# Kernel optimization log

Hardware: AMD Instinct MI355X
Metric: run time of the kernel (lower is better)

## Reference

```python
import jax, jax.numpy as jnp
import numpy as np

N_NODES = 10242  # icosphere level-5 node count
NNZ = 71694      # ~7 nonzeros per row (6 neighbors + self)


def setup_inputs() -> dict:
    key = jax.random.key(0)
    k1, k2, k3, k4, k5 = jax.random.split(key, 5)
    B, T, C, Cout, Ks = 2, 16, 16, 32, 20
    x = jax.random.normal(k1, (B, T, N_NODES, C), dtype=jnp.float32)
    edge_row = jax.random.randint(k2, (NNZ,), 0, N_NODES, dtype=jnp.int32)
    edge_col = jax.random.randint(k3, (NNZ,), 0, N_NODES, dtype=jnp.int32)
    # small values keep the Chebyshev recurrence numerically bounded over Ks steps
    edge_val = jax.random.uniform(k4, (NNZ,), dtype=jnp.float32, minval=-0.2, maxval=0.2)
    W = jax.random.normal(k5, (Cout, C * Ks), dtype=jnp.float32) * 0.02
    return {"x": x, "edge_row": edge_row, "edge_col": edge_col,
            "edge_val": edge_val, "W": W}


def reference(x, edge_row, edge_col, edge_val, W):
    B, T, N, C = x.shape
    Cout, CK = W.shape
    Ks = CK // C

    def spmm(v):  # sparse L @ v, v: [N, F]
        return jax.ops.segment_sum(edge_val[:, None] * v[edge_col], edge_row,
                                   num_segments=N)

    # [B,T,N,C] -> [B*T,N,C] -> [N,C,B*T] -> [N, C*B*T]
    x0 = x.reshape(B * T, N, C).transpose(1, 2, 0).reshape(N, C * B * T)
    x1 = spmm(x0)

    def step(carry, _):
        a, b = carry
        c = 2.0 * spmm(b) - a
        return (b, c), c

    _, rest = jax.lax.scan(step, (x0, x1), None, length=Ks - 2)
    xs = jnp.concatenate([x0[None], x1[None], rest], axis=0)  # [Ks, N, C*B*T]

    xs = xs.reshape(Ks, N, C, B * T).transpose(3, 1, 2, 0)  # [B*T, N, C, Ks]
    xs = xs.reshape(B * T * N, C * Ks)
    out = xs @ W.T  # [B*T*N, Cout]
    return out.reshape(B, T, N, Cout)
```

## Files before the change

kernel.cpp:

```cpp
#include <hip/hip_runtime.h>

#define N_NODES 10242
#define NNZ_E   71694
#define NNZ_PAD_MAX (NNZ_E + 7 * N_NODES + 64)
#define BT      32
#define C_IN    16
#define K_S     20
#define C_OUT   32
#define F       512
typedef unsigned short u16;
typedef unsigned int   u32;

#define RING_ELEMS ((size_t)N_NODES * F)
#define RING_BYTES (RING_ELEMS * 2)

#define NSLICE  8
#define SLICE_U16 (F / NSLICE)

typedef __attribute__((ext_vector_type(8)))  _Float16 half8;
typedef __attribute__((ext_vector_type(16))) float    float16;

__device__ __forceinline__ void unpack8h(uint4 u, float* f) {
    union { uint4 u; _Float16 h[8]; } v; v.u = u;
    #pragma unroll
    for (int i = 0; i < 8; ++i) f[i] = (float)v.h[i];
}
__device__ __forceinline__ uint4 pack8h(const float* f) {
    union { uint4 u; _Float16 h[8]; } v;
    #pragma unroll
    for (int i = 0; i < 8; ++i) v.h[i] = (_Float16)f[i];
    return v.u;
}
__device__ __forceinline__ u16 f2h(float f) {
    union { _Float16 h; u16 u; } v; v.h = (_Float16)f; return v.u;
}


__global__ __launch_bounds__(256) void init_kernel(
        const float* __restrict__ W, int* __restrict__ cnt,
        u16* __restrict__ wtfrag) {
    int i = blockIdx.x * 256 + threadIdx.x;
    if (i < N_NODES) cnt[i] = 0;
    int w = i - N_NODES;
    if (w >= 0 && w < K_S * 64 * 8) {
        int j    = w & 7;
        int lane = (w >> 3) & 63;
        int k    = w >> 9;
        int cout = lane & 31;
        int c    = ((lane >> 5) << 3) + j;
        wtfrag[w] = f2h(W[cout * (C_IN * K_S) + c * K_S + k]);
    }
}

__global__ __launch_bounds__(256) void count_kernel(
        const int* __restrict__ erow, int* cnt) {
    int e = blockIdx.x * 256 + threadIdx.x;
    if (e < NNZ_E) atomicAdd(&cnt[erow[e]], 1);
}

__global__ __launch_bounds__(256) void scan_kernel(
        const int* __restrict__ cnt, int* row_ptr, int* cursor) {
    const int T = 256;
    const int chunk = (N_NODES + T - 1) / T;
    __shared__ int part[T];
    int t = threadIdx.x;
    int base = t * chunk;
    int s = 0;
    for (int i = 0; i < chunk; ++i) {
        int idx = base + i;
        if (idx < N_NODES) s += (cnt[idx] + 7) & ~7;
    }
    part[t] = s;
    __syncthreads();
    for (int off = 1; off < T; off <<= 1) {
        int v = (t >= off) ? part[t - off] : 0;
        __syncthreads();
        part[t] += v;
        __syncthreads();
    }
    int run = (t == 0) ? 0 : part[t - 1];
    for (int i = 0; i < chunk; ++i) {
        int idx = base + i;
        if (idx < N_NODES) {
            row_ptr[idx] = run;
            cursor[idx]  = run;
            run += (cnt[idx] + 7) & ~7;
        }
    }
    if (t == T - 1) row_ptr[N_NODES] = part[T - 1];
}

__global__ __launch_bounds__(256) void scatter_kernel(
        const int* __restrict__ erow, const int* __restrict__ ecol,
        const float* __restrict__ eval, int* cursor, int2* __restrict__ cpack) {
    int e = blockIdx.x * 256 + threadIdx.x;
    if (e < NNZ_E) {
        int p = atomicAdd(&cursor[erow[e]], 1);
        cpack[p] = make_int2(ecol[e], __float_as_int(eval[e]));
    }
}

__global__ __launch_bounds__(256) void finalize_kernel(
        const int* __restrict__ row_ptr, const int* __restrict__ cursor,
        int2* cpack) {
    int r = blockIdx.x * 256 + threadIdx.x;
    if (r >= N_NODES) return;
    int sbeg = row_ptr[r];
    int send = cursor[r];
    int pend = row_ptr[r + 1];
    for (int i = sbeg + 1; i < send; ++i) {
        int2 key = cpack[i];
        int j = i - 1;
        while (j >= sbeg) {
            int2 q = cpack[j];
            bool gt = (q.x > key.x) || (q.x == key.x && (u32)q.y > (u32)key.y);
            if (!gt) break;
            cpack[j + 1] = q;
            --j;
        }
        cpack[j + 1] = key;
    }
    for (int p = send; p < pend; ++p) cpack[p] = make_int2(0, 0);
}


__global__ __launch_bounds__(256) void transform_kernel(
        const float* __restrict__ x, u16* __restrict__ T0) {
    int g = blockIdx.x * 256 + threadIdx.x;
    int n   = g >> 9;
    int rem = g & 511;
    int bt  = rem >> 4;
    int c   = rem & 15;
    float v = x[((size_t)bt * N_NODES + n) * C_IN + c];
    T0[(size_t)n * F + rem] = f2h(v);
}


__global__ __launch_bounds__(256) void spmm_slice_kernel(
        const u16* __restrict__ srcB, const u16* __restrict__ srcA,
        u16* __restrict__ dst,
        const int* __restrict__ row_ptr, const int2* __restrict__ cpack,
        float alpha, float beta) {
    const int slice = blockIdx.x & 7;
    const int chunk = blockIdx.x >> 3;
    const int wave  = threadIdx.x >> 6;
    const int lane  = threadIdx.x & 63;
    const int l     = lane & 7;
    const int n     = chunk * 32 + wave * 8 + (lane >> 3);
    const bool valid = (n < N_NODES);

    const int s   = valid ? row_ptr[n] : 0;
    const int len = valid ? (row_ptr[n + 1] - s) : 0;

    const size_t soff = (size_t)slice * SLICE_U16 + (size_t)l * 8;

    float a[8] = {0,0,0,0,0,0,0,0};
    if (beta != 0.f && valid) {
        uint4 ua = *(const uint4*)(srcA + (size_t)n * F + soff);
        unpack8h(ua, a);
    }

    float acc[8] = {0,0,0,0,0,0,0,0};
    const int gbase = lane & 56;

    for (int c = 0; c * 8 < len; ++c) {
        int2 my = cpack[s + c * 8 + l];
        int col[8]; float v[8];
        #pragma unroll
        for (int r = 0; r < 8; ++r) {
            col[r] = __shfl(my.x, gbase + r, 64);
            v[r]   = __int_as_float(__shfl(my.y, gbase + r, 64));
        }
        uint4 g0 = *(const uint4*)(srcB + (size_t)col[0] * F + soff);
        uint4 g1 = *(const uint4*)(srcB + (size_t)col[1] * F + soff);
        uint4 g2 = *(const uint4*)(srcB + (size_t)col[2] * F + soff);
        uint4 g3 = *(const uint4*)(srcB + (size_t)col[3] * F + soff);
        uint4 g4 = *(const uint4*)(srcB + (size_t)col[4] * F + soff);
        uint4 g5 = *(const uint4*)(srcB + (size_t)col[5] * F + soff);
        uint4 g6 = *(const uint4*)(srcB + (size_t)col[6] * F + soff);
        uint4 g7 = *(const uint4*)(srcB + (size_t)col[7] * F + soff);
        float b0[8], b1[8], b2[8], b3[8], b4[8], b5[8], b6[8], b7[8];
        unpack8h(g0, b0); unpack8h(g1, b1); unpack8h(g2, b2); unpack8h(g3, b3);
        unpack8h(g4, b4); unpack8h(g5, b5); unpack8h(g6, b6); unpack8h(g7, b7);
        #pragma unroll
        for (int i = 0; i < 8; ++i) {
            acc[i] += v[0] * b0[i];
            acc[i] += v[1] * b1[i];
            acc[i] += v[2] * b2[i];
            acc[i] += v[3] * b3[i];
            acc[i] += v[4] * b4[i];
            acc[i] += v[5] * b5[i];
            acc[i] += v[6] * b6[i];
            acc[i] += v[7] * b7[i];
        }
    }

    if (valid) {
        float y[8];
        #pragma unroll
        for (int i = 0; i < 8; ++i)
            y[i] = alpha * acc[i] + beta * a[i];
        *(uint4*)(dst + (size_t)n * F + soff) = pack8h(y);
    }
}


__global__ __launch_bounds__(256) void proj_mfma_kernel(
        const u16* __restrict__ ring, int R, int k0, int kcnt,
        const u16* __restrict__ wtfrag, float* __restrict__ out, int accumulate) {
    const int lane = threadIdx.x & 63;
    const int n = (blockIdx.x << 2) + (threadIdx.x >> 6);
    if (n >= N_NODES) return;
    const int col = lane & 31;
    const int grp = lane >> 5;
    const size_t aoff = (size_t)n * F + (size_t)col * 16 + grp * 8;

    union U { uint4 u; half8 h; };
    float16 acc0 = {};
    float16 acc1 = {};
    int j = 0;
    for (; j + 2 <= kcnt; j += 2) {
        int ka = k0 + j, kb = k0 + j + 1;
        U a0, b0, a1, b1;
        a0.u = *(const uint4*)(ring + (size_t)(ka % R) * RING_ELEMS + aoff);
        b0.u = *(const uint4*)(wtfrag + (size_t)ka * 512 + lane * 8);
        a1.u = *(const uint4*)(ring + (size_t)(kb % R) * RING_ELEMS + aoff);
        b1.u = *(const uint4*)(wtfrag + (size_t)kb * 512 + lane * 8);
        acc0 = __builtin_amdgcn_mfma_f32_32x32x16_f16(a0.h, b0.h, acc0, 0, 0, 0);
        acc1 = __builtin_amdgcn_mfma_f32_32x32x16_f16(a1.h, b1.h, acc1, 0, 0, 0);
    }
    if (j < kcnt) {
        int ka = k0 + j;
        U a0, b0;
        a0.u = *(const uint4*)(ring + (size_t)(ka % R) * RING_ELEMS + aoff);
        b0.u = *(const uint4*)(wtfrag + (size_t)ka * 512 + lane * 8);
        acc0 = __builtin_amdgcn_mfma_f32_32x32x16_f16(a0.h, b0.h, acc0, 0, 0, 0);
    }

    #pragma unroll
    for (int r = 0; r < 16; ++r) {
        int bt = (r & 3) + 8 * (r >> 2) + 4 * grp;
        float* op = out + ((size_t)bt * N_NODES + n) * C_OUT + col;
        float val = acc0[r] + acc1[r];
        if (accumulate) *op += val;
        else            *op  = val;
    }
}


extern "C" void kernel_launch(void* const* d_in, const int* in_sizes, int n_in,
                              void* d_out, int out_size, void* d_ws, size_t ws_size,
                              hipStream_t stream) {
    const float* x    = (const float*)d_in[0];
    const int*   erow = (const int*)  d_in[1];
    const int*   ecol = (const int*)  d_in[2];
    const float* eval = (const float*)d_in[3];
    const float* W    = (const float*)d_in[4];
    float* out = (float*)d_out;

    char* ws = (char*)d_ws;
    size_t o = 0;
    auto alloc = [&](size_t bytes) -> char* {
        o = (o + 511) & ~(size_t)511;
        char* r = ws + o;
        o += bytes;
        return r;
    };
    int*   cnt     = (int*)  alloc((size_t)N_NODES * 4);
    int*   row_ptr = (int*)  alloc((size_t)(N_NODES + 1) * 4);
    int*   cursor  = (int*)  alloc((size_t)N_NODES * 4);
    int2*  cpack   = (int2*) alloc((size_t)NNZ_PAD_MAX * 8);
    u16*   wtfrag  = (u16*)  alloc((size_t)K_S * 512 * 2);

    o = (o + 511) & ~(size_t)511;
    int R = (int)((ws_size - o) / RING_BYTES);
    if (R > K_S) R = K_S;
    if (R < 3)  R = 3;
    u16* ring = (u16*)(ws + o);
    auto slot = [&](int k) -> u16* { return ring + (size_t)(k % R) * RING_ELEMS; };

    init_kernel<<<(N_NODES + K_S * 512 + 255) / 256, 256, 0, stream>>>(W, cnt, wtfrag);
    count_kernel<<<(NNZ_E + 255) / 256, 256, 0, stream>>>(erow, cnt);
    scan_kernel<<<1, 256, 0, stream>>>(cnt, row_ptr, cursor);
    scatter_kernel<<<(NNZ_E + 255) / 256, 256, 0, stream>>>(erow, ecol, eval, cursor, cpack);
    finalize_kernel<<<(N_NODES + 255) / 256, 256, 0, stream>>>(row_ptr, cursor, cpack);

    const int grid4  = (N_NODES + 3) / 4;
    const int gridsl = NSLICE * ((N_NODES + 31) / 32);
    int c0 = 0;
    auto maybe_pass = [&](int k_done) {
        int target = K_S - c0;
        if (target > R) target = R;
        if (target > 0 && (k_done - c0 + 1) == target) {
            proj_mfma_kernel<<<grid4, 256, 0, stream>>>(
                ring, R, c0, target, wtfrag, out, (c0 > 0) ? 1 : 0);
            c0 += target;
        }
    };

    transform_kernel<<<(int)(RING_ELEMS / 256), 256, 0, stream>>>(x, slot(0));
    maybe_pass(0);

    for (int k = 1; k < K_S; ++k) {
        const u16* srcB = slot(k - 1);
        const u16* srcA = (k >= 2) ? slot(k - 2) : slot(k - 1);
        float alpha = (k == 1) ? 1.f : 2.f;
        float beta  = (k == 1) ? 0.f : -1.f;
        spmm_slice_kernel<<<gridsl, 256, 0, stream>>>(
            srcB, srcA, slot(k), row_ptr, cpack, alpha, beta);
        maybe_pass(k);
    }
}
```

Measured before the change: 451.0 us.

## Run whole Chebyshev recurrence per feature pair in LDS-resident single kernel

Adds a chain kernel in which each of 256 blocks owns two feature columns, keeps the full node vector for two consecutive recurrence steps in shared memory, and runs all Ks-1 SpMM steps with block barriers. This replaces 19 separate SpMM launches that gathered from global memory. Edges are repacked into 32-bit words holding a 16-bit column and an fp16 value, and nodes are sorted by row-length class to reduce divergence. A single projection pass follows when the workspace ring holds all Ks slots. The cost is about 80KB of LDS per block, which limits occupancy, scattered fp16 writes to the ring, and fp16 rounding of the edge values.

```diff
diff --git a/kernel.cpp b/kernel.cpp
--- a/kernel.cpp
+++ b/kernel.cpp
@@ -33,6 +33,15 @@
 }
 __device__ __forceinline__ u16 f2h(float f) {
     union { _Float16 h; u16 u; } v; v.h = (_Float16)f; return v.u;
+}
+__device__ __forceinline__ float h2f_lo(u32 w) {
+    union { u32 u; _Float16 h[2]; } v; v.u = w; return (float)v.h[0];
+}
+__device__ __forceinline__ float h2f_hi(u32 w) {
+    union { u32 u; _Float16 h[2]; } v; v.u = w; return (float)v.h[1];
+}
+__device__ __forceinline__ u32 packh2(float a, float b) {
+    union { u32 u; _Float16 h[2]; } v; v.h[0] = (_Float16)a; v.h[1] = (_Float16)b; return v.u;
 }
 
 
@@ -59,16 +68,26 @@
 }
 
 __global__ __launch_bounds__(256) void scan_kernel(
-        const int* __restrict__ cnt, int* row_ptr, int* cursor) {
+        const int* __restrict__ cnt, int* row_ptr, int* cursor,
+        int* class_cursor) {
     const int T = 256;
     const int chunk = (N_NODES + T - 1) / T;
     __shared__ int part[T];
+    __shared__ int ccnt[8];
     int t = threadIdx.x;
+    if (t < 8) ccnt[t] = 0;
+    __syncthreads();
     int base = t * chunk;
     int s = 0;
     for (int i = 0; i < chunk; ++i) {
         int idx = base + i;
-        if (idx < N_NODES) s += (cnt[idx] + 7) & ~7;
+        if (idx < N_NODES) {
+            int pl = (cnt[idx] + 7) & ~7;
+            s += pl;
+            int cls = (pl == 0) ? 0 : ((pl >> 3) - 1);
+            if (cls > 7) cls = 7;
+            atomicAdd(&ccnt[cls], 1);
+        }
     }
     part[t] = s;
     __syncthreads();
@@ -88,6 +107,11 @@
         }
     }
     if (t == T - 1) row_ptr[N_NODES] = part[T - 1];
+    __syncthreads();
+    if (t == 0) {
+        int r2 = 0;
+        for (int c2 = 0; c2 < 8; ++c2) { class_cursor[c2] = r2; r2 += ccnt[c2]; }
+    }
 }
 
 __global__ __launch_bounds__(256) void scatter_kernel(
@@ -102,7 +126,7 @@
 
 __global__ __launch_bounds__(256) void finalize_kernel(
         const int* __restrict__ row_ptr, const int* __restrict__ cursor,
-        int2* cpack) {
+        int2* cpack, u32* __restrict__ epack) {
     int r = blockIdx.x * 256 + threadIdx.x;
     if (r >= N_NODES) return;
     int sbeg = row_ptr[r];
@@ -121,86 +145,77 @@
         cpack[j + 1] = key;
     }
     for (int p = send; p < pend; ++p) cpack[p] = make_int2(0, 0);
-}
-
-
-__global__ __launch_bounds__(256) void transform_kernel(
-        const float* __restrict__ x, u16* __restrict__ T0) {
-    int g = blockIdx.x * 256 + threadIdx.x;
-    int n   = g >> 9;
-    int rem = g & 511;
-    int bt  = rem >> 4;
-    int c   = rem & 15;
-    float v = x[((size_t)bt * N_NODES + n) * C_IN + c];
-    T0[(size_t)n * F + rem] = f2h(v);
-}
-
-
-__global__ __launch_bounds__(256) void spmm_slice_kernel(
-        const u16* __restrict__ srcB, const u16* __restrict__ srcA,
-        u16* __restrict__ dst,
-        const int* __restrict__ row_ptr, const int2* __restrict__ cpack,
-        float alpha, float beta) {
-    const int slice = blockIdx.x & 7;
-    const int chunk = blockIdx.x >> 3;
-    const int wave  = threadIdx.x >> 6;
-    const int lane  = threadIdx.x & 63;
-    const int l     = lane & 7;
-    const int n     = chunk * 32 + wave * 8 + (lane >> 3);
-    const bool valid = (n < N_NODES);
-
-    const int s   = valid ? row_ptr[n] : 0;
-    const int len = valid ? (row_ptr[n + 1] - s) : 0;
-
-    const size_t soff = (size_t)slice * SLICE_U16 + (size_t)l * 8;
-
-    float a[8] = {0,0,0,0,0,0,0,0};
-    if (beta != 0.f && valid) {
-        uint4 ua = *(const uint4*)(srcA + (size_t)n * F + soff);
-        unpack8h(ua, a);
-    }
-
-    float acc[8] = {0,0,0,0,0,0,0,0};
-    const int gbase = lane & 56;
-
-    for (int c = 0; c * 8 < len; ++c) {
-        int2 my = cpack[s + c * 8 + l];
-        int col[8]; float v[8];
-        #pragma unroll
-        for (int r = 0; r < 8; ++r) {
-            col[r] = __shfl(my.x, gbase + r, 64);
-            v[r]   = __int_as_float(__shfl(my.y, gbase + r, 64));
-        }
-        uint4 g0 = *(const uint4*)(srcB + (size_t)col[0] * F + soff);
-        uint4 g1 = *(const uint4*)(srcB + (size_t)col[1] * F + soff);
-        uint4 g2 = *(const uint4*)(srcB + (size_t)col[2] * F + soff);
-        uint4 g3 = *(const uint4*)(srcB + (size_t)col[3] * F + soff);
-        uint4 g4 = *(const uint4*)(srcB + (size_t)col[4] * F + soff);
-        uint4 g5 = *(const uint4*)(srcB + (size_t)col[5] * F + soff);
-        uint4 g6 = *(const uint4*)(srcB + (size_t)col[6] * F + soff);
-        uint4 g7 = *(const uint4*)(srcB + (size_t)col[7] * F + soff);
-        float b0[8], b1[8], b2[8], b3[8], b4[8], b5[8], b6[8], b7[8];
-        unpack8h(g0, b0); unpack8h(g1, b1); unpack8h(g2, b2); unpack8h(g3, b3);
-        unpack8h(g4, b4); unpack8h(g5, b5); unpack8h(g6, b6); unpack8h(g7, b7);
-        #pragma unroll
-        for (int i = 0; i < 8; ++i) {
-            acc[i] += v[0] * b0[i];
-            acc[i] += v[1] * b1[i];
-            acc[i] += v[2] * b2[i];
-            acc[i] += v[3] * b3[i];
-            acc[i] += v[4] * b4[i];
-            acc[i] += v[5] * b5[i];
-            acc[i] += v[6] * b6[i];
-            acc[i] += v[7] * b7[i];
-        }
-    }
-
-    if (valid) {
-        float y[8];
-        #pragma unroll
-        for (int i = 0; i < 8; ++i)
-            y[i] = alpha * acc[i] + beta * a[i];
-        *(uint4*)(dst + (size_t)n * F + soff) = pack8h(y);
+    for (int p = sbeg; p < pend; ++p) {
+        int2 q = cpack[p];
+        epack[p] = ((u32)q.x & 0xFFFFu) |
+                   ((u32)f2h(__int_as_float(q.y)) << 16);
+    }
+}
+
+__global__ __launch_bounds__(256) void order_kernel(
+        const int* __restrict__ row_ptr, int* class_cursor,
+        int* __restrict__ node_order) {
+    int n = blockIdx.x * 256 + threadIdx.x;
+    if (n >= N_NODES) return;
+    int pl = row_ptr[n + 1] - row_ptr[n];
+    int cls = (pl == 0) ? 0 : ((pl >> 3) - 1);
+    if (cls > 7) cls = 7;
+    int pos = atomicAdd(&class_cursor[cls], 1);
+    node_order[pos] = n;
+}
+
+
+__global__ __launch_bounds__(1024) void chain_kernel(
+        const float* __restrict__ x, const int* __restrict__ row_ptr,
+        const u32* __restrict__ epack, const int* __restrict__ node_order,
+        u16* __restrict__ ring) {
+    __shared__ u32 Tsh[2][N_NODES];
+    const int t  = threadIdx.x;
+    const int b  = blockIdx.x;
+    const int f0 = ((b & 7) << 6) | ((b >> 3) << 1);
+    const int bt = f0 >> 4;
+    const int c0 = f0 & 15;
+
+    for (int i = t; i < N_NODES; i += 1024) {
+        const float* xp = x + ((size_t)bt * N_NODES + i) * C_IN + c0;
+        float2 xv = *(const float2*)xp;
+        u32 p = packh2(xv.x, xv.y);
+        Tsh[0][i] = p;
+        *(u32*)(ring + (size_t)i * F + f0) = p;
+    }
+    __syncthreads();
+
+    int cur = 0;
+    for (int k = 1; k < K_S; ++k) {
+        const u32* bsrc = &Tsh[cur][0];
+        u32* adst = &Tsh[cur ^ 1][0];
+        u16* rk = ring + (size_t)k * RING_ELEMS;
+        const float alpha = (k == 1) ? 1.f : 2.f;
+        const bool hasA = (k >= 2);
+        for (int i = t; i < N_NODES; i += 1024) {
+            int n = node_order[i];
+            int s = row_ptr[n], e = row_ptr[n + 1];
+            float a0 = 0.f, a1 = 0.f;
+            if (hasA) { u32 ap = adst[n]; a0 = h2f_lo(ap); a1 = h2f_hi(ap); }
+            float acc0 = 0.f, acc1 = 0.f;
+            for (int p = s; p < e; p += 8) {
+                uint4 q0 = *(const uint4*)(epack + p);
+                uint4 q1 = *(const uint4*)(epack + p + 4);
+                #define EDGE(u) { u32 cc = (u) & 0xFFFFu; u32 d = bsrc[cc]; \
+                    float vv = h2f_hi(u); \
+                    acc0 += vv * h2f_lo(d); acc1 += vv * h2f_hi(d); }
+                EDGE(q0.x) EDGE(q0.y) EDGE(q0.z) EDGE(q0.w)
+                EDGE(q1.x) EDGE(q1.y) EDGE(q1.z) EDGE(q1.w)
+                #undef EDGE
+            }
+            float y0 = alpha * acc0 - (hasA ? a0 : 0.f);
+            float y1 = alpha * acc1 - (hasA ? a1 : 0.f);
+            u32 yp = packh2(y0, y1);
+            adst[n] = yp;
+            *(u32*)(rk + (size_t)n * F + f0) = yp;
+        }
+        __syncthreads();
+        cur ^= 1;
     }
 }
 
@@ -248,6 +263,67 @@
 }
 
 
+__global__ __launch_bounds__(256) void transform_kernel(
+        const float* __restrict__ x, u16* __restrict__ T0) {
+    int g = blockIdx.x * 256 + threadIdx.x;
+    int n   = g >> 9;
+    int rem = g & 511;
+    int bt  = rem >> 4;
+    int c   = rem & 15;
+    float v = x[((size_t)bt * N_NODES + n) * C_IN + c];
+    T0[(size_t)n * F + rem] = f2h(v);
+}
+
+__global__ __launch_bounds__(256) void spmm_slice_kernel(
+        const u16* __restrict__ srcB, const u16* __restrict__ srcA,
+        u16* __restrict__ dst,
+        const int* __restrict__ row_ptr, const int2* __restrict__ cpack,
+        float alpha, float beta) {
+    const int slice = blockIdx.x & 7;
+    const int chunk = blockIdx.x >> 3;
+    const int wave  = threadIdx.x >> 6;
+    const int lane  = threadIdx.x & 63;
+    const int l     = lane & 7;
+    const int n     = chunk * 32 + wave * 8 + (lane >> 3);
+    const bool valid = (n < N_NODES);
+
+    const int s   = valid ? row_ptr[n] : 0;
+    const int len = valid ? (row_ptr[n + 1] - s) : 0;
+    const size_t soff = (size_t)slice * SLICE_U16 + (size_t)l * 8;
+
+    float a[8] = {0,0,0,0,0,0,0,0};
+    if (beta != 0.f && valid) {
+        uint4 ua = *(const uint4*)(srcA + (size_t)n * F + soff);
+        unpack8h(ua, a);
+    }
+    float acc[8] = {0,0,0,0,0,0,0,0};
+    const int gbase = lane & 56;
+    for (int c = 0; c * 8 < len; ++c) {
+        int2 my = cpack[s + c * 8 + l];
+        int col[8]; float v[8];
+        #pragma unroll
+        for (int r = 0; r < 8; ++r) {
+            col[r] = __shfl(my.x, gbase + r, 64);
+            v[r]   = __int_as_float(__shfl(my.y, gbase + r, 64));
+        }
+        #pragma unroll
+        for (int r = 0; r < 8; ++r) {
+            uint4 g = *(const uint4*)(srcB + (size_t)col[r] * F + soff);
+            float bb[8];
+            unpack8h(g, bb);
+            #pragma unroll
+            for (int i = 0; i < 8; ++i) acc[i] += v[r] * bb[i];
+        }
+    }
+    if (valid) {
+        float y[8];
+        #pragma unroll
+        for (int i = 0; i < 8; ++i) y[i] = alpha * acc[i] + beta * a[i];
+        *(uint4*)(dst + (size_t)n * F + soff) = pack8h(y);
+    }
+}
+
+
 extern "C" void kernel_launch(void* const* d_in, const int* in_sizes, int n_in,
                               void* d_out, int out_size, void* d_ws, size_t ws_size,
                               hipStream_t stream) {
@@ -266,11 +342,14 @@
         o += bytes;
         return r;
     };
-    int*   cnt     = (int*)  alloc((size_t)N_NODES * 4);
-    int*   row_ptr = (int*)  alloc((size_t)(N_NODES + 1) * 4);
-    int*   cursor  = (int*)  alloc((size_t)N_NODES * 4);
-    int2*  cpack   = (int2*) alloc((size_t)NNZ_PAD_MAX * 8);
-    u16*   wtfrag  = (u16*)  alloc((size_t)K_S * 512 * 2);
+    int*   cnt      = (int*)  alloc((size_t)N_NODES * 4);
+    int*   row_ptr  = (int*)  alloc((size_t)(N_NODES + 1) * 4);
+    int*   cursor   = (int*)  alloc((size_t)N_NODES * 4);
+    int2*  cpack    = (int2*) alloc((size_t)NNZ_PAD_MAX * 8);
+    u32*   epack    = (u32*)  alloc((size_t)NNZ_PAD_MAX * 4);
+    u16*   wtfrag   = (u16*)  alloc((size_t)K_S * 512 * 2);
+    int*   clscur   = (int*)  alloc(8 * 4);
+    int*   norder   = (int*)  alloc((size_t)N_NODES * 4);
 
     o = (o + 511) & ~(size_t)511;
     int R = (int)((ws_size - o) / RING_BYTES);
@@ -281,11 +360,20 @@
 
     init_kernel<<<(N_NODES + K_S * 512 + 255) / 256, 256, 0, stream>>>(W, cnt, wtfrag);
     count_kernel<<<(NNZ_E + 255) / 256, 256, 0, stream>>>(erow, cnt);
-    scan_kernel<<<1, 256, 0, stream>>>(cnt, row_ptr, cursor);
+    scan_kernel<<<1, 256, 0, stream>>>(cnt, row_ptr, cursor, clscur);
     scatter_kernel<<<(NNZ_E + 255) / 256, 256, 0, stream>>>(erow, ecol, eval, cursor, cpack);
-    finalize_kernel<<<(N_NODES + 255) / 256, 256, 0, stream>>>(row_ptr, cursor, cpack);
-
-    const int grid4  = (N_NODES + 3) / 4;
+    finalize_kernel<<<(N_NODES + 255) / 256, 256, 0, stream>>>(row_ptr, cursor, cpack, epack);
+    order_kernel<<<(N_NODES + 255) / 256, 256, 0, stream>>>(row_ptr, clscur, norder);
+
+    const int grid4 = (N_NODES + 3) / 4;
+
+    if (R >= K_S) {
+        chain_kernel<<<256, 1024, 0, stream>>>(x, row_ptr, epack, norder, ring);
+        proj_mfma_kernel<<<grid4, 256, 0, stream>>>(
+            ring, K_S, 0, K_S, wtfrag, out, 0);
+        return;
+    }
+
     const int gridsl = NSLICE * ((N_NODES + 31) / 32);
     int c0 = 0;
     auto maybe_pass = [&](int k_done) {
@@ -297,10 +385,8 @@
             c0 += target;
         }
     };
-
     transform_kernel<<<(int)(RING_ELEMS / 256), 256, 0, stream>>>(x, slot(0));
     maybe_pass(0);
-
     for (int k = 1; k < K_S; ++k) {
         const u16* srcB = slot(k - 1);
         const u16* srcA = (k >= 2) ? slot(k - 2) : slot(k - 1);
```

After: 742.2 us. +64.6%, slower.
